# Kernel tuning notes

Measured on AMD Instinct MI355X. Metric: run time of the kernel, lower is better.

## Reference

```python
import jax, jax.numpy as jnp
import numpy as np

P = 16
D = 768          # latent_dim
H = 3072         # hidden_dim
B = 256
OUT_DIMS = [100 + 10 * i for i in range(P)]   # sum = 2800
MAX_OUT = max(OUT_DIMS)
EPS = 1e-5


def setup_inputs() -> dict:
    key = jax.random.key(0)
    ks = jax.random.split(key, 6)
    x = jax.random.normal(ks[0], (B, P, D), dtype=jnp.float32)
    # LayerNorm params per part (torch default init: gamma=1, beta=0)
    gamma = jnp.ones((P, D), dtype=jnp.float32)
    beta = jnp.zeros((P, D), dtype=jnp.float32)
    # fc1: Linear(D, H, bias=False) per part -> stacked [P, H, D]
    w1 = jax.random.normal(ks[1], (P, H, D), dtype=jnp.float32) * 0.02
    # fc2: Linear(H, out_dims[i], bias=True) per part, padded to MAX_OUT.
    # Padded rows are never read (sliced away at concat).
    w2 = jax.random.normal(ks[2], (P, MAX_OUT, H), dtype=jnp.float32) * 0.02
    b2 = jnp.zeros((P, MAX_OUT), dtype=jnp.float32)
    return {"x": x, "gamma": gamma, "beta": beta, "w1": w1, "w2": w2, "b2": b2}


def reference(x, gamma, beta, w1, w2, b2):
    # Per-part LayerNorm over latent dim (torch uses biased variance)
    mu = jnp.mean(x, axis=-1, keepdims=True)
    var = jnp.mean(jnp.square(x - mu), axis=-1, keepdims=True)
    xn = (x - mu) * jax.lax.rsqrt(var + EPS) * gamma[None] + beta[None]  # [B,P,D]
    # fc1 (no bias) + exact GELU (torch.nn.GELU default)
    h = jnp.einsum('bpd,phd->bph', xn, w1)          # [B,P,H]
    h = jax.nn.gelu(h, approximate=False)
    # dropout p=0.0 -> identity
    # fc2 (with bias), padded grouped GEMM
    out_full = jnp.einsum('bph,poh->bpo', h, w2) + b2[None]  # [B,P,MAX_OUT]
    # concat variable-width slices along last dim
    out = jnp.concatenate([out_full[:, i, :OUT_DIMS[i]] for i in range(P)], axis=-1)
    return out  # [B, sum(OUT_DIMS)] = [256, 2800]
```

## Files before the change

kernel.cpp:

```cpp
#include <hip/hip_runtime.h>
#include <math.h>

typedef unsigned short u16;
typedef unsigned int u32;
typedef __attribute__((ext_vector_type(4))) float f32x4;
typedef __attribute__((ext_vector_type(8))) short bf16x8;

#define NP 16
#define DLAT 768
#define HDIM 3072
#define NB 256
#define MAXO 250
#define TOT 2800

__device__ __forceinline__ u16 f2b(float f) {
  union { float f; u32 u; } v; v.f = f;
  u32 u = v.u;
  u32 r = (u + 0x7fffu + ((u >> 16) & 1u)) >> 16;
  return (u16)r;
}

__device__ __forceinline__ void gll16(const void* g, void* l) {
  __builtin_amdgcn_global_load_lds(
      (const __attribute__((address_space(1))) void*)g,
      (__attribute__((address_space(3))) void*)l, 16, 0, 0);
}

__global__ __launch_bounds__(256) void ln_kernel(
    const float* __restrict__ x, const float* __restrict__ gamma,
    const float* __restrict__ beta, u16* __restrict__ xn) {
  const int wave = threadIdx.x >> 6, lane = threadIdx.x & 63;
  const int row = blockIdx.x * 4 + wave;
  const int b = row >> 4, p = row & 15;
  const float4* xr = (const float4*)(x + (size_t)row * DLAT);
  const float4* g4 = (const float4*)(gamma + (size_t)p * DLAT);
  const float4* b4 = (const float4*)(beta + (size_t)p * DLAT);
  float4 v[3];
  float s = 0.f, ss = 0.f;
#pragma unroll
  for (int j = 0; j < 3; ++j) {
    v[j] = xr[lane + j * 64];
    s += v[j].x + v[j].y + v[j].z + v[j].w;
    ss += v[j].x * v[j].x + v[j].y * v[j].y + v[j].z * v[j].z + v[j].w * v[j].w;
  }
#pragma unroll
  for (int o = 32; o; o >>= 1) { s += __shfl_xor(s, o); ss += __shfl_xor(ss, o); }
  const float mu = s * (1.f / 768.f);
  const float var = ss * (1.f / 768.f) - mu * mu;
  const float rstd = rsqrtf(var + 1e-5f);
  u16* xo = xn + ((size_t)(p * NB + b)) * DLAT;
#pragma unroll
  for (int j = 0; j < 3; ++j) {
    const int f = lane + j * 64;
    float4 g = g4[f], be = b4[f];
    float o0 = (v[j].x - mu) * rstd * g.x + be.x;
    float o1 = (v[j].y - mu) * rstd * g.y + be.y;
    float o2 = (v[j].z - mu) * rstd * g.z + be.z;
    float o3 = (v[j].w - mu) * rstd * g.w + be.w;
    uint2 w;
    w.x = (u32)f2b(o0) | ((u32)f2b(o1) << 16);
    w.y = (u32)f2b(o2) | ((u32)f2b(o3) << 16);
    *(uint2*)&xo[f * 4] = w;
  }
}

__global__ __launch_bounds__(256, 2) void fc1_kernel(
    const u16* __restrict__ xn, const float* __restrict__ w1, u16* __restrict__ h) {
  const int bid = blockIdx.x;
  const int bs = (bid & 7) * 96 + (bid >> 3);
  const int p = bs / 48;
  const int n0 = (bs % 48) * 64;
  const int tid = threadIdx.x;
  const int lane = tid & 63, wave = tid >> 6;
  const int lanelo = lane & 15, lanehi = lane >> 4;

  const u16* Ap = xn + (size_t)p * NB * DLAT;
  const float* Bp = w1 + (size_t)p * HDIM * DLAT + (size_t)n0 * DLAT;

  __shared__ u16 As[3][256 * 32];
  __shared__ u16 Bs[2][64 * 32];

  int ag_off[4];
  const int ag_base = (256 * wave) * 8;
#pragma unroll
  for (int i = 0; i < 4; ++i) {
    int slot = 256 * wave + 64 * i + lane;
    int r = slot >> 2;
    int c = (slot & 3) ^ ((r >> 1) & 3);
    ag_off[i] = r * DLAT + c * 8;
  }
  const float* bg0 = Bp + (size_t)(tid >> 3) * DLAT + (tid & 7) * 4;
  const float* bg1 = bg0 + (size_t)32 * DLAT;
  int bso[2];
#pragma unroll
  for (int i = 0; i < 2; ++i) {
    int r = (tid >> 3) + 32 * i;
    int c = ((tid & 7) >> 1) ^ ((r >> 1) & 3);
    bso[i] = (r * 4 + c) * 8 + (tid & 1) * 4;
  }
  int a_sl[4], b_sl[4];
#pragma unroll
  for (int m = 0; m < 4; ++m) {
    int r = wave * 64 + m * 16 + lanelo;
    a_sl[m] = (r * 4 + (lanehi ^ ((r >> 1) & 3))) * 8;
    int rb = m * 16 + lanelo;
    b_sl[m] = (rb * 4 + (lanehi ^ ((rb >> 1) & 3))) * 8;
  }

  f32x4 acc[4][4] = {};
  float4 bA0, bA1, bB0, bB1;
  const int NK = DLAT / 32;

  auto issue = [&](int kt, float4& r0, float4& r1) {
    const int k2 = kt * 32;
    u16* lb = &As[kt % 3][ag_base];
#pragma unroll
    for (int i = 0; i < 4; ++i) gll16(Ap + ag_off[i] + k2, lb + i * 512);
    asm volatile("" ::: "memory");
    r0 = *(const float4*)(bg0 + k2);
    r1 = *(const float4*)(bg1 + k2);
    asm volatile("" ::: "memory");
  };

  auto step = [&](int kt, float4& r0, float4& r1) {
    if (kt + 1 < NK) asm volatile("s_waitcnt vmcnt(6)" ::: "memory");
    else             asm volatile("s_waitcnt vmcnt(0)" ::: "memory");
    {
      u16* bb = &Bs[kt & 1][0];
      uint2 w0, w1v;
      w0.x = (u32)f2b(r0.x) | ((u32)f2b(r0.y) << 16);
      w0.y = (u32)f2b(r0.z) | ((u32)f2b(r0.w) << 16);
      w1v.x = (u32)f2b(r1.x) | ((u32)f2b(r1.y) << 16);
      w1v.y = (u32)f2b(r1.z) | ((u32)f2b(r1.w) << 16);
      *(uint2*)&bb[bso[0]] = w0;
      *(uint2*)&bb[bso[1]] = w1v;
    }
    asm volatile("s_waitcnt lgkmcnt(0)" ::: "memory");
    __builtin_amdgcn_s_barrier();
    asm volatile("" ::: "memory");
    if (kt + 2 < NK) issue(kt + 2, r0, r1);
    const u16* a_ = &As[kt % 3][0];
    const u16* b_ = &Bs[kt & 1][0];
    bf16x8 af[4], bf[4];
#pragma unroll
    for (int m = 0; m < 4; ++m) af[m] = *(const bf16x8*)&a_[a_sl[m]];
#pragma unroll
    for (int n = 0; n < 4; ++n) bf[n] = *(const bf16x8*)&b_[b_sl[n]];
#pragma unroll
    for (int m = 0; m < 4; ++m)
#pragma unroll
      for (int n = 0; n < 4; ++n)
        acc[m][n] = __builtin_amdgcn_mfma_f32_16x16x32_bf16(af[m], bf[n], acc[m][n], 0, 0, 0);
  };

  issue(0, bA0, bA1);
  issue(1, bB0, bB1);
  for (int kt = 0; kt < NK; kt += 2) {
    step(kt, bA0, bA1);
    step(kt + 1, bB0, bB1);
  }

  u16* hp = h + (size_t)p * NB * HDIM;
#pragma unroll
  for (int m = 0; m < 4; ++m) {
#pragma unroll
    for (int n = 0; n < 4; ++n) {
      const int col = n0 + n * 16 + lanelo;
#pragma unroll
      for (int r = 0; r < 4; ++r) {
        const int row = wave * 64 + m * 16 + lanehi * 4 + r;
        const float vv = acc[m][n][r];
        const float gel = 0.5f * vv * (1.f + erff(vv * 0.70710678118654752f));
        hp[(size_t)row * HDIM + col] = f2b(gel);
      }
    }
  }
}

__global__ __launch_bounds__(256) void fc2_kernel(
    const u16* __restrict__ hbuf, const float* __restrict__ w2,
    const float* __restrict__ b2, float* __restrict__ out) {
  const int bid = blockIdx.x;
  const int bs = (bid & 7) * 32 + (bid >> 3);
  const int p = bs >> 4;
  const int mb = (bs >> 2) & 3;
  const int nb = bs & 3;
  const int odim = 100 + 10 * p;
  const int n0 = nb * 64;
  if (n0 >= odim) return;
  const int m0 = mb * 64;
  const int off = 100 * p + 5 * p * (p - 1);

  const int tid = threadIdx.x;
  const int lane = tid & 63, wave = tid >> 6;
  const int lanelo = lane & 15, lanehi = lane >> 4;
  const int wr = wave >> 1, wc = wave & 1;

  const u16* Ap = hbuf + (size_t)p * NB * HDIM + (size_t)m0 * HDIM;
  const float* Bp = w2 + (size_t)p * MAXO * HDIM;

  __shared__ u16 As[3][64 * 32];
  __shared__ u16 Bs[2][64 * 32];

  int ag_off;
  const int ag_base = (64 * wave) * 8;
  {
    int slot = 64 * wave + lane;
    int r = slot >> 2;
    int c = (slot & 3) ^ ((r >> 1) & 3);
    ag_off = r * HDIM + c * 8;
  }
  const int br0 = min(n0 + (tid >> 3), MAXO - 1);
  const int br1 = min(n0 + (tid >> 3) + 32, MAXO - 1);
  const float* bg0 = Bp + (size_t)br0 * HDIM + (tid & 7) * 4;
  const float* bg1 = Bp + (size_t)br1 * HDIM + (tid & 7) * 4;
  int bso[2];
#pragma unroll
  for (int i = 0; i < 2; ++i) {
    int r = (tid >> 3) + 32 * i;
    int c = ((tid & 7) >> 1) ^ ((r >> 1) & 3);
    bso[i] = (r * 4 + c) * 8 + (tid & 1) * 4;
  }
  int a_sl[2], b_sl[2];
#pragma unroll
  for (int m = 0; m < 2; ++m) {
    int r = wr * 32 + m * 16 + lanelo;
    a_sl[m] = (r * 4 + (lanehi ^ ((r >> 1) & 3))) * 8;
    int rb = wc * 32 + m * 16 + lanelo;
    b_sl[m] = (rb * 4 + (lanehi ^ ((rb >> 1) & 3))) * 8;
  }

  f32x4 acc[2][2] = {};
  float4 bA0, bA1, bB0, bB1;
  const int NK = HDIM / 32;

  auto issue = [&](int kt, float4& r0, float4& r1) {
    const int k2 = kt * 32;
    gll16(Ap + ag_off + k2, &As[kt % 3][ag_base]);
    asm volatile("" ::: "memory");
    r0 = *(const float4*)(bg0 + k2);
    r1 = *(const float4*)(bg1 + k2);
    asm volatile("" ::: "memory");
  };

  auto step = [&](int kt, float4& r0, float4& r1) {
    if (kt + 1 < NK) asm volatile("s_waitcnt vmcnt(3)" ::: "memory");
    else             asm volatile("s_waitcnt vmcnt(0)" ::: "memory");
    {
      u16* bb = &Bs[kt & 1][0];
      uint2 w0, w1v;
      w0.x = (u32)f2b(r0.x) | ((u32)f2b(r0.y) << 16);
      w0.y = (u32)f2b(r0.z) | ((u32)f2b(r0.w) << 16);
      w1v.x = (u32)f2b(r1.x) | ((u32)f2b(r1.y) << 16);
      w1v.y = (u32)f2b(r1.z) | ((u32)f2b(r1.w) << 16);
      *(uint2*)&bb[bso[0]] = w0;
      *(uint2*)&bb[bso[1]] = w1v;
    }
    asm volatile("s_waitcnt lgkmcnt(0)" ::: "memory");
    __builtin_amdgcn_s_barrier();
    asm volatile("" ::: "memory");
    if (kt + 2 < NK) issue(kt + 2, r0, r1);
    const u16* a_ = &As[kt % 3][0];
    const u16* b_ = &Bs[kt & 1][0];
    bf16x8 af[2], bf[2];
#pragma unroll
    for (int m = 0; m < 2; ++m) af[m] = *(const bf16x8*)&a_[a_sl[m]];
#pragma unroll
    for (int n = 0; n < 2; ++n) bf[n] = *(const bf16x8*)&b_[b_sl[n]];
#pragma unroll
    for (int m = 0; m < 2; ++m)
#pragma unroll
      for (int n = 0; n < 2; ++n)
        acc[m][n] = __builtin_amdgcn_mfma_f32_16x16x32_bf16(af[m], bf[n], acc[m][n], 0, 0, 0);
  };

  issue(0, bA0, bA1);
  issue(1, bB0, bB1);
  for (int kt = 0; kt < NK; kt += 2) {
    step(kt, bA0, bA1);
    step(kt + 1, bB0, bB1);
  }

#pragma unroll
  for (int m = 0; m < 2; ++m) {
#pragma unroll
    for (int n = 0; n < 2; ++n) {
      const int col = n0 + wc * 32 + n * 16 + lanelo;
      if (col < odim) {
        const float bias = b2[(size_t)p * MAXO + col];
#pragma unroll
        for (int r = 0; r < 4; ++r) {
          const int row = m0 + wr * 32 + m * 16 + lanehi * 4 + r;
          out[(size_t)row * TOT + off + col] = acc[m][n][r] + bias;
        }
      }
    }
  }
}

extern "C" void kernel_launch(void* const* d_in, const int* in_sizes, int n_in,
                              void* d_out, int out_size, void* d_ws, size_t ws_size,
                              hipStream_t stream) {
  const float* x = (const float*)d_in[0];
  const float* gamma = (const float*)d_in[1];
  const float* beta = (const float*)d_in[2];
  const float* w1 = (const float*)d_in[3];
  const float* w2 = (const float*)d_in[4];
  const float* b2 = (const float*)d_in[5];
  float* out = (float*)d_out;

  u16* xn = (u16*)d_ws;
  u16* h = (u16*)d_ws + (size_t)NP * NB * DLAT;

  ln_kernel<<<1024, 256, 0, stream>>>(x, gamma, beta, xn);
  fc1_kernel<<<NP * 48, 256, 0, stream>>>(xn, w1, h);
  fc2_kernel<<<NP * 16, 256, 0, stream>>>(h, w2, b2, out);
}
```

Before: 109.4 us.

## Load fc1 operands directly from global into registers, dropping LDS staging

The fc1 kernel no longer stages A and B tiles through shared memory. Each lane now loads its MFMA fragments straight from global memory into registers, double-buffered in registers, and converts w1 to bf16 with the packed v_cvt_pk_bf16_f32 instruction. This removes LDS writes, reads and swizzle bookkeeping, but gives up intra-block data sharing: each wave reloads the same B columns, and A rows are read by every block. The block-index remap for cache locality and the two-blocks-per-CU launch bound are also removed.

```diff
diff --git a/kernel.cpp b/kernel.cpp
--- a/kernel.cpp
+++ b/kernel.cpp
@@ -20,10 +20,10 @@
   return (u16)r;
 }
 
-__device__ __forceinline__ void gll16(const void* g, void* l) {
-  __builtin_amdgcn_global_load_lds(
-      (const __attribute__((address_space(1))) void*)g,
-      (__attribute__((address_space(3))) void*)l, 16, 0, 0);
+__device__ __forceinline__ u32 cvtpk(float lo, float hi) {
+  u32 r;
+  asm("v_cvt_pk_bf16_f32 %0, %1, %2" : "=v"(r) : "v"(lo), "v"(hi));
+  return r;
 }
 
 __global__ __launch_bounds__(256) void ln_kernel(
@@ -64,100 +64,69 @@
   }
 }
 
-__global__ __launch_bounds__(256, 2) void fc1_kernel(
+__global__ __launch_bounds__(256) void fc1_kernel(
     const u16* __restrict__ xn, const float* __restrict__ w1, u16* __restrict__ h) {
   const int bid = blockIdx.x;
-  const int bs = (bid & 7) * 96 + (bid >> 3);
-  const int p = bs / 48;
-  const int n0 = (bs % 48) * 64;
+  const int p = bid / 48;
+  const int n0 = (bid % 48) * 64;
   const int tid = threadIdx.x;
   const int lane = tid & 63, wave = tid >> 6;
   const int lanelo = lane & 15, lanehi = lane >> 4;
 
-  const u16* Ap = xn + (size_t)p * NB * DLAT;
-  const float* Bp = w1 + (size_t)p * HDIM * DLAT + (size_t)n0 * DLAT;
-
-  __shared__ u16 As[3][256 * 32];
-  __shared__ u16 Bs[2][64 * 32];
-
-  int ag_off[4];
-  const int ag_base = (256 * wave) * 8;
-#pragma unroll
-  for (int i = 0; i < 4; ++i) {
-    int slot = 256 * wave + 64 * i + lane;
-    int r = slot >> 2;
-    int c = (slot & 3) ^ ((r >> 1) & 3);
-    ag_off[i] = r * DLAT + c * 8;
-  }
-  const float* bg0 = Bp + (size_t)(tid >> 3) * DLAT + (tid & 7) * 4;
-  const float* bg1 = bg0 + (size_t)32 * DLAT;
-  int bso[2];
-#pragma unroll
-  for (int i = 0; i < 2; ++i) {
-    int r = (tid >> 3) + 32 * i;
-    int c = ((tid & 7) >> 1) ^ ((r >> 1) & 3);
-    bso[i] = (r * 4 + c) * 8 + (tid & 1) * 4;
-  }
-  int a_sl[4], b_sl[4];
-#pragma unroll
-  for (int m = 0; m < 4; ++m) {
-    int r = wave * 64 + m * 16 + lanelo;
-    a_sl[m] = (r * 4 + (lanehi ^ ((r >> 1) & 3))) * 8;
-    int rb = m * 16 + lanelo;
-    b_sl[m] = (rb * 4 + (lanehi ^ ((rb >> 1) & 3))) * 8;
-  }
+  const u16* Ap = xn + (size_t)p * NB * DLAT
+                  + (size_t)(wave * 64 + lanelo) * DLAT + lanehi * 8;
+  const float* Bp = w1 + (size_t)p * HDIM * DLAT
+                    + (size_t)(n0 + lanelo) * DLAT + lanehi * 8;
 
   f32x4 acc[4][4] = {};
-  float4 bA0, bA1, bB0, bB1;
+  bf16x8 a0[4], a1[4];
+  float4 b0[4][2], b1[4][2];
+
+  auto LDA = [&](bf16x8* a, int k) {
+#pragma unroll
+    for (int m = 0; m < 4; ++m)
+      a[m] = *(const bf16x8*)(Ap + (size_t)m * 16 * DLAT + k);
+  };
+  auto LDB = [&](float4 (*b)[2], int k) {
+#pragma unroll
+    for (int n = 0; n < 4; ++n) {
+      const float* q = Bp + (size_t)n * 16 * DLAT + k;
+      b[n][0] = *(const float4*)q;
+      b[n][1] = *(const float4*)(q + 4);
+    }
+  };
+  auto FMAS = [&](bf16x8* a, float4 (*b)[2]) {
+    bf16x8 fb[4];
+#pragma unroll
+    for (int n = 0; n < 4; ++n) {
+      union { u32 u[4]; bf16x8 v; } t;
+      t.u[0] = cvtpk(b[n][0].x, b[n][0].y);
+      t.u[1] = cvtpk(b[n][0].z, b[n][0].w);
+      t.u[2] = cvtpk(b[n][1].x, b[n][1].y);
+      t.u[3] = cvtpk(b[n][1].z, b[n][1].w);
+      fb[n] = t.v;
+    }
+#pragma unroll
+    for (int m = 0; m < 4; ++m)
+#pragma unroll
+      for (int n = 0; n < 4; ++n)
+        acc[m][n] = __builtin_amdgcn_mfma_f32_16x16x32_bf16(a[m], fb[n], acc[m][n], 0, 0, 0);
+  };
+
+  LDA(a0, 0);
+  LDB(b0, 0);
   const int NK = DLAT / 32;
-
-  auto issue = [&](int kt, float4& r0, float4& r1) {
-    const int k2 = kt * 32;
-    u16* lb = &As[kt % 3][ag_base];
-#pragma unroll
-    for (int i = 0; i < 4; ++i) gll16(Ap + ag_off[i] + k2, lb + i * 512);
-    asm volatile("" ::: "memory");
-    r0 = *(const float4*)(bg0 + k2);
-    r1 = *(const float4*)(bg1 + k2);
-    asm volatile("" ::: "memory");
-  };
-
-  auto step = [&](int kt, float4& r0, float4& r1) {
-    if (kt + 1 < NK) asm volatile("s_waitcnt vmcnt(6)" ::: "memory");
-    else             asm volatile("s_waitcnt vmcnt(0)" ::: "memory");
-    {
-      u16* bb = &Bs[kt & 1][0];
-      uint2 w0, w1v;
-      w0.x = (u32)f2b(r0.x) | ((u32)f2b(r0.y) << 16);
-      w0.y = (u32)f2b(r0.z) | ((u32)f2b(r0.w) << 16);
-      w1v.x = (u32)f2b(r1.x) | ((u32)f2b(r1.y) << 16);
-      w1v.y = (u32)f2b(r1.z) | ((u32)f2b(r1.w) << 16);
-      *(uint2*)&bb[bso[0]] = w0;
-      *(uint2*)&bb[bso[1]] = w1v;
-    }
-    asm volatile("s_waitcnt lgkmcnt(0)" ::: "memory");
+  for (int kt = 0; kt < NK; kt += 2) {
+    LDA(a1, (kt + 1) * 32);
+    LDB(b1, (kt + 1) * 32);
     __builtin_amdgcn_s_barrier();
-    asm volatile("" ::: "memory");
-    if (kt + 2 < NK) issue(kt + 2, r0, r1);
-    const u16* a_ = &As[kt % 3][0];
-    const u16* b_ = &Bs[kt & 1][0];
-    bf16x8 af[4], bf[4];
-#pragma unroll
-    for (int m = 0; m < 4; ++m) af[m] = *(const bf16x8*)&a_[a_sl[m]];
-#pragma unroll
-    for (int n = 0; n < 4; ++n) bf[n] = *(const bf16x8*)&b_[b_sl[n]];
-#pragma unroll
-    for (int m = 0; m < 4; ++m)
-#pragma unroll
-      for (int n = 0; n < 4; ++n)
-        acc[m][n] = __builtin_amdgcn_mfma_f32_16x16x32_bf16(af[m], bf[n], acc[m][n], 0, 0, 0);
-  };
-
-  issue(0, bA0, bA1);
-  issue(1, bB0, bB1);
-  for (int kt = 0; kt < NK; kt += 2) {
-    step(kt, bA0, bA1);
-    step(kt + 1, bB0, bB1);
+    FMAS(a0, b0);
+    if (kt + 2 < NK) {
+      LDA(a0, (kt + 2) * 32);
+      LDB(b0, (kt + 2) * 32);
+    }
+    __builtin_amdgcn_s_barrier();
+    FMAS(a1, b1);
   }
 
   u16* hp = h + (size_t)p * NB * HDIM;
@@ -234,6 +203,12 @@
   float4 bA0, bA1, bB0, bB1;
   const int NK = HDIM / 32;
 
+  auto gll16 = [](const void* g, void* l) {
+    __builtin_amdgcn_global_load_lds(
+        (const __attribute__((address_space(1))) void*)g,
+        (__attribute__((address_space(3))) void*)l, 16, 0, 0);
+  };
+
   auto issue = [&](int kt, float4& r0, float4& r1) {
     const int k2 = kt * 32;
     gll16(Ap + ag_off + k2, &As[kt % 3][ag_base]);
```

After: 162.0 us. 1.48x slower.

## Split fc1 M dimension into 64-row tiles with deeper 4-stage prefetch

Applied to the files above, without the earlier changes.

The fc1 kernel now tiles the 256-row batch into four 64-row blocks, launching four times as many workgroups. Each wave computes a 32x32 sub-tile laid out on a 2x2 wave grid instead of 64x64. The A-tile LDS ring grows to 5 stages and the prefetch distance to 4 k-steps, with graded vmcnt waits in the tail. The aim is more parallelism and better latency hiding. The cost is that each w1 tile is now read, and converted from fp32 to bf16, four times instead of once, which raises weight traffic and conversion work.

```diff
diff --git a/kernel.cpp b/kernel.cpp
--- a/kernel.cpp
+++ b/kernel.cpp
@@ -64,30 +64,35 @@
   }
 }
 
-__global__ __launch_bounds__(256, 2) void fc1_kernel(
+__global__ __launch_bounds__(256) void fc1_kernel(
     const u16* __restrict__ xn, const float* __restrict__ w1, u16* __restrict__ h) {
   const int bid = blockIdx.x;
-  const int bs = (bid & 7) * 96 + (bid >> 3);
-  const int p = bs / 48;
-  const int n0 = (bs % 48) * 64;
+  const int xcd = bid & 7;
+  const int q = bid >> 3;
+  const int g = xcd * 96 + (q >> 2);
+  const int mb = q & 3;
+  const int p = g / 48;
+  const int nb = g % 48;
+  const int m0 = mb * 64, n0 = nb * 64;
+
   const int tid = threadIdx.x;
   const int lane = tid & 63, wave = tid >> 6;
   const int lanelo = lane & 15, lanehi = lane >> 4;
-
-  const u16* Ap = xn + (size_t)p * NB * DLAT;
+  const int wr = wave >> 1, wc = wave & 1;
+
+  const u16* Ap = xn + (size_t)p * NB * DLAT + (size_t)m0 * DLAT;
   const float* Bp = w1 + (size_t)p * HDIM * DLAT + (size_t)n0 * DLAT;
 
-  __shared__ u16 As[3][256 * 32];
+  __shared__ u16 As[5][64 * 32];
   __shared__ u16 Bs[2][64 * 32];
 
-  int ag_off[4];
-  const int ag_base = (256 * wave) * 8;
-#pragma unroll
-  for (int i = 0; i < 4; ++i) {
-    int slot = 256 * wave + 64 * i + lane;
+  int ag_off;
+  const int ag_base = (64 * wave) * 8;
+  {
+    int slot = 64 * wave + lane;
     int r = slot >> 2;
     int c = (slot & 3) ^ ((r >> 1) & 3);
-    ag_off[i] = r * DLAT + c * 8;
+    ag_off = r * DLAT + c * 8;
   }
   const float* bg0 = Bp + (size_t)(tid >> 3) * DLAT + (tid & 7) * 4;
   const float* bg1 = bg0 + (size_t)32 * DLAT;
@@ -98,35 +103,36 @@
     int c = ((tid & 7) >> 1) ^ ((r >> 1) & 3);
     bso[i] = (r * 4 + c) * 8 + (tid & 1) * 4;
   }
-  int a_sl[4], b_sl[4];
-#pragma unroll
-  for (int m = 0; m < 4; ++m) {
-    int r = wave * 64 + m * 16 + lanelo;
+  int a_sl[2], b_sl[2];
+#pragma unroll
+  for (int m = 0; m < 2; ++m) {
+    int r = wr * 32 + m * 16 + lanelo;
     a_sl[m] = (r * 4 + (lanehi ^ ((r >> 1) & 3))) * 8;
-    int rb = m * 16 + lanelo;
+    int rb = wc * 32 + m * 16 + lanelo;
     b_sl[m] = (rb * 4 + (lanehi ^ ((rb >> 1) & 3))) * 8;
   }
 
-  f32x4 acc[4][4] = {};
-  float4 bA0, bA1, bB0, bB1;
+  f32x4 acc[2][2] = {};
+  float4 rB[4][2];
   const int NK = DLAT / 32;
 
-  auto issue = [&](int kt, float4& r0, float4& r1) {
+  auto issue = [&](int kt) {
     const int k2 = kt * 32;
-    u16* lb = &As[kt % 3][ag_base];
-#pragma unroll
-    for (int i = 0; i < 4; ++i) gll16(Ap + ag_off[i] + k2, lb + i * 512);
-    asm volatile("" ::: "memory");
-    r0 = *(const float4*)(bg0 + k2);
-    r1 = *(const float4*)(bg1 + k2);
+    gll16(Ap + ag_off + k2, &As[kt % 5][ag_base]);
+    asm volatile("" ::: "memory");
+    rB[kt & 3][0] = *(const float4*)(bg0 + k2);
+    rB[kt & 3][1] = *(const float4*)(bg1 + k2);
     asm volatile("" ::: "memory");
   };
 
-  auto step = [&](int kt, float4& r0, float4& r1) {
-    if (kt + 1 < NK) asm volatile("s_waitcnt vmcnt(6)" ::: "memory");
-    else             asm volatile("s_waitcnt vmcnt(0)" ::: "memory");
+  auto step = [&](int kt, int wn) {
+    if (wn == 9)      asm volatile("s_waitcnt vmcnt(9)" ::: "memory");
+    else if (wn == 6) asm volatile("s_waitcnt vmcnt(6)" ::: "memory");
+    else if (wn == 3) asm volatile("s_waitcnt vmcnt(3)" ::: "memory");
+    else              asm volatile("s_waitcnt vmcnt(0)" ::: "memory");
     {
       u16* bb = &Bs[kt & 1][0];
+      const float4 r0 = rB[kt & 3][0], r1 = rB[kt & 3][1];
       uint2 w0, w1v;
       w0.x = (u32)f2b(r0.x) | ((u32)f2b(r0.y) << 16);
       w0.y = (u32)f2b(r0.z) | ((u32)f2b(r0.w) << 16);
@@ -138,37 +144,37 @@
     asm volatile("s_waitcnt lgkmcnt(0)" ::: "memory");
     __builtin_amdgcn_s_barrier();
     asm volatile("" ::: "memory");
-    if (kt + 2 < NK) issue(kt + 2, r0, r1);
-    const u16* a_ = &As[kt % 3][0];
+    if (kt + 4 < NK) issue(kt + 4);
+    const u16* a_ = &As[kt % 5][0];
     const u16* b_ = &Bs[kt & 1][0];
-    bf16x8 af[4], bf[4];
-#pragma unroll
-    for (int m = 0; m < 4; ++m) af[m] = *(const bf16x8*)&a_[a_sl[m]];
-#pragma unroll
-    for (int n = 0; n < 4; ++n) bf[n] = *(const bf16x8*)&b_[b_sl[n]];
-#pragma unroll
-    for (int m = 0; m < 4; ++m)
-#pragma unroll
-      for (int n = 0; n < 4; ++n)
+    bf16x8 af[2], bf[2];
+#pragma unroll
+    for (int m = 0; m < 2; ++m) af[m] = *(const bf16x8*)&a_[a_sl[m]];
+#pragma unroll
+    for (int n = 0; n < 2; ++n) bf[n] = *(const bf16x8*)&b_[b_sl[n]];
+#pragma unroll
+    for (int m = 0; m < 2; ++m)
+#pragma unroll
+      for (int n = 0; n < 2; ++n)
         acc[m][n] = __builtin_amdgcn_mfma_f32_16x16x32_bf16(af[m], bf[n], acc[m][n], 0, 0, 0);
   };
 
-  issue(0, bA0, bA1);
-  issue(1, bB0, bB1);
-  for (int kt = 0; kt < NK; kt += 2) {
-    step(kt, bA0, bA1);
-    step(kt + 1, bB0, bB1);
-  }
+  issue(0); issue(1); issue(2); issue(3);
+#pragma unroll
+  for (int kt = 0; kt < NK - 3; ++kt) step(kt, 9);
+  step(NK - 3, 6);
+  step(NK - 2, 3);
+  step(NK - 1, 0);
 
   u16* hp = h + (size_t)p * NB * HDIM;
 #pragma unroll
-  for (int m = 0; m < 4; ++m) {
-#pragma unroll
-    for (int n = 0; n < 4; ++n) {
-      const int col = n0 + n * 16 + lanelo;
+  for (int m = 0; m < 2; ++m) {
+#pragma unroll
+    for (int n = 0; n < 2; ++n) {
+      const int col = n0 + wc * 32 + n * 16 + lanelo;
 #pragma unroll
       for (int r = 0; r < 4; ++r) {
-        const int row = wave * 64 + m * 16 + lanehi * 4 + r;
+        const int row = m0 + wr * 32 + m * 16 + lanehi * 4 + r;
         const float vv = acc[m][n][r];
         const float gel = 0.5f * vv * (1.f + erff(vv * 0.70710678118654752f));
         hp[(size_t)row * HDIM + col] = f2b(gel);
@@ -313,6 +319,6 @@
   u16* h = (u16*)d_ws + (size_t)NP * NB * DLAT;
 
   ln_kernel<<<1024, 256, 0, stream>>>(x, gamma, beta, xn);
-  fc1_kernel<<<NP * 48, 256, 0, stream>>>(xn, w1, h);
+  fc1_kernel<<<NP * 48 * 4, 256, 0, stream>>>(xn, w1, h);
   fc2_kernel<<<NP * 16, 256, 0, stream>>>(h, w2, b2, out);
 }
```

Result: slower. 127.6 us (+16.7%).
